# Kernel optimization log

Measured on AMD Instinct MI355X. Metric: run time of the kernel, lower is better.

The kernel has to match this reference:

```python
import jax, jax.numpy as jnp
import numpy as np

H, W, BS, CIN = 224, 608, 1, 128
CLS = (16, 12, 10)
PAD = (0, 2, 3)
C12 = CLS[0] * CLS[1]            # 192
C123 = C12 * CLS[2]              # 1920
SUPER = 384
CFACT = C123 // SUPER            # 5
PAD_PROJ = 0.1


def _p(key, shape):
    return jax.random.normal(key, shape, dtype=jnp.float32) * 0.05


def setup_inputs() -> dict:
    key = jax.random.key(0)
    ks = iter(jax.random.split(key, 32))
    d = {"x_in": jax.random.normal(next(ks), (BS, CIN, H, W), dtype=jnp.float32)}
    # stage-1: grouped 1x1 convs (groups=height -> one [out,in] matmul per image line)
    for i, (ci, co) in enumerate([(32, 32), (32, 32), (32, CLS[0] + 2 * PAD[0])]):
        d[f"w1_{i}"] = _p(next(ks), (H, co, ci))
        d[f"b1_{i}"] = _p(next(ks), (H, co))
    # stage-2: CondMul tables indexed by line*16 + stage-1 class
    for i, (ci, co) in enumerate([(32, 32), (32, 32), (32, CLS[1] + 2 * PAD[1])]):
        d[f"w2_{i}"] = _p(next(ks), (H * CLS[0], ci, co))
        d[f"b2_{i}"] = _p(next(ks), (H * CLS[0], co))
    # stage-3: CondMul tables indexed by line*192 + stage-12 class
    for i, (ci, co) in enumerate([(32, 32), (32, 32), (32, CLS[2] + 2 * PAD[2])]):
        d[f"w3_{i}"] = _p(next(ks), (H * C12, ci, co))
        d[f"b3_{i}"] = _p(next(ks), (H * C12, co))
    d["wr0"] = _p(next(ks), (H * SUPER, 32, 32))
    d["br0"] = _p(next(ks), (H * SUPER, 32))
    d["wr1"] = _p(next(ks), (H * C123, 32, 1))
    d["br1"] = _p(next(ks), (H * C123, 1))
    return d


def _condmul(x, inds, w, b):
    # CondMul: y[n] = x[n] @ w[inds[n]] + b[inds[n]]
    return jnp.einsum('ni,nio->no', x, w[inds]) + b[inds]


def _forward(x_in, w1, b1, w2, b2, w3, b3, wr0, br0, wr1, br1):
    bs, _, h, w_ = x_in.shape
    lrelu = jax.nn.leaky_relu  # negative_slope=0.01, same as torch default
    offsets = jnp.arange(h, dtype=jnp.int32).reshape(1, 1, h, 1)
    # ---- stage 1: per-line 1x1 grouped conv stack -> argmax class
    x = x_in[:, 0:32].transpose(0, 2, 1, 3)                    # [b,h,32,w]
    for i in range(3):
        x = jnp.einsum('bhiw,hoi->bhow', x, w1[i]) + b1[i][None, :, :, None]
        if i < 2:
            x = lrelu(x)
    x = x.transpose(0, 2, 1, 3)                                 # [b,16,h,w]
    inds1 = jnp.argmax(x, axis=1)[:, None].astype(jnp.int32)    # [b,1,h,w]
    inds1_l = (inds1 + CLS[0] * offsets).reshape(-1)
    # ---- stage 2: CondMul chain conditioned on (line, class1)
    x = x_in[:, 32:64].transpose(0, 2, 3, 1).reshape(-1, 32)    # [N,32]
    for i in range(3):
        x = _condmul(x, inds1_l, w2[i], b2[i])
        if i < 2:
            x = lrelu(x)
    inds2 = jnp.argmax(x, axis=1).astype(jnp.int32).reshape(bs, 1, h, w_)
    inds12 = inds1 * CLS[1] + (inds2 - PAD[1])
    inds12_l = (jnp.clip(inds12, 0, C12 - 1) + C12 * offsets).reshape(-1)
    # ---- stage 3: CondMul chain conditioned on (line, class12)
    x = x_in[:, 64:96].transpose(0, 2, 3, 1).reshape(-1, 32)
    for i in range(3):
        if i < 2:
            x = lrelu(_condmul(x, inds12_l, w3[i], b3[i]))
        else:
            x = _condmul(x, inds12_l, w3[i], b3[i])
    inds3 = jnp.argmax(x, axis=1).astype(jnp.int32).reshape(bs, 1, h, w_)
    inds123 = jnp.clip(inds12 * CLS[2] + (inds3 - PAD[2]), 0, C123 - 1)
    inds = inds123.reshape(-1)
    lines = jnp.broadcast_to(offsets, (bs, 1, h, w_)).reshape(-1)
    inds_l = inds + C123 * lines                                 # per-leaf index
    inds_super_l = inds // CFACT + SUPER * lines                 # superclass index (reg_line_div=1)
    x = x_in[:, 96:128].transpose(0, 2, 3, 1).reshape(-1, 32)
    x = lrelu(_condmul(x, inds_super_l, wr0, br0))
    r = _condmul(x, inds_l, wr1, br1)[:, 0]                      # [N]
    out = (inds.astype(jnp.float32) + r).reshape(bs, 1, h, w_) / float(C123)
    out = (out - PAD_PROJ) / (1.0 - 2.0 * PAD_PROJ)              # undo projector padding
    return out


def reference(x_in, w1_0, b1_0, w1_1, b1_1, w1_2, b1_2,
              w2_0, b2_0, w2_1, b2_1, w2_2, b2_2,
              w3_0, b3_0, w3_1, b3_1, w3_2, b3_2,
              wr0, br0, wr1, br1):
    return _forward(x_in,
                    (w1_0, w1_1, w1_2), (b1_0, b1_1, b1_2),
                    (w2_0, w2_1, w2_2), (b2_0, b2_1, b2_2),
                    (w3_0, w3_1, w3_2), (b3_0, b3_1, b3_2),
                    wr0, br0, wr1, br1)
```

## Files before the change

kernel.cpp:

```cpp
#include <hip/hip_runtime.h>
#include <cstddef>

#define HH 224
#define WW 608
#define HWSZ (HH * WW)

__device__ __forceinline__ float lrelu(float v) { return v > 0.0f ? v : 0.01f * v; }

template <int CO>
__device__ __forceinline__ void cm4(const float* __restrict__ wmat,
                                    const float* __restrict__ bvec,
                                    int s, const float (&act)[8], float (&acc)[CO / 4]) {
    constexpr int CH = CO / 4;
#pragma unroll
    for (int j = 0; j < CH; j++) acc[j] = 0.0f;
#pragma unroll
    for (int sp = 0; sp < 4; sp++) {
#pragma unroll
        for (int ii = 0; ii < 8; ii++) {
            float xi = __shfl(act[ii], sp, 4);
            const float* wr = wmat + (sp * 8 + ii) * CO + s * CH;
            if constexpr (CH == 8) {
                float4 a = *reinterpret_cast<const float4*>(wr);
                float4 b = *reinterpret_cast<const float4*>(wr + 4);
                acc[0] = fmaf(xi, a.x, acc[0]); acc[1] = fmaf(xi, a.y, acc[1]);
                acc[2] = fmaf(xi, a.z, acc[2]); acc[3] = fmaf(xi, a.w, acc[3]);
                acc[4] = fmaf(xi, b.x, acc[4]); acc[5] = fmaf(xi, b.y, acc[5]);
                acc[6] = fmaf(xi, b.z, acc[6]); acc[7] = fmaf(xi, b.w, acc[7]);
            } else {
                float4 a = *reinterpret_cast<const float4*>(wr);
                acc[0] = fmaf(xi, a.x, acc[0]); acc[1] = fmaf(xi, a.y, acc[1]);
                acc[2] = fmaf(xi, a.z, acc[2]); acc[3] = fmaf(xi, a.w, acc[3]);
            }
        }
    }
#pragma unroll
    for (int j = 0; j < CH; j++) acc[j] += bvec[s * CH + j];
}

__device__ __forceinline__ void wb_lrelu8(float (&act)[8], const float (&acc)[8]) {
#pragma unroll
    for (int j = 0; j < 8; j++) act[j] = lrelu(acc[j]);
}

__device__ __forceinline__ int argmax4(const float (&v)[4], int s) {
    float bv = v[0];
    int bi = 4 * s;
#pragma unroll
    for (int j = 1; j < 4; j++) {
        if (v[j] > bv) { bv = v[j]; bi = 4 * s + j; }
    }
#pragma unroll
    for (int m = 1; m <= 2; m <<= 1) {
        float ov = __shfl_xor(bv, m, 4);
        int oi = __shfl_xor(bi, m, 4);
        if (ov > bv || (ov == bv && oi < bi)) { bv = ov; bi = oi; }
    }
    return bi;
}

extern "C" __global__ __launch_bounds__(256, 4)
void regressor_fused(const float* __restrict__ x_in,
                     const float* __restrict__ w1_0, const float* __restrict__ b1_0,
                     const float* __restrict__ w1_1, const float* __restrict__ b1_1,
                     const float* __restrict__ w1_2, const float* __restrict__ b1_2,
                     const float* __restrict__ w2_0, const float* __restrict__ b2_0,
                     const float* __restrict__ w2_1, const float* __restrict__ b2_1,
                     const float* __restrict__ w2_2, const float* __restrict__ b2_2,
                     const float* __restrict__ w3_0, const float* __restrict__ b3_0,
                     const float* __restrict__ w3_1, const float* __restrict__ b3_1,
                     const float* __restrict__ w3_2, const float* __restrict__ b3_2,
                     const float* __restrict__ wr0, const float* __restrict__ br0,
                     const float* __restrict__ wr1, const float* __restrict__ br1,
                     float* __restrict__ out) {
    const int h = blockIdx.y;
    const int tid = threadIdx.x;
    const int p = tid >> 2;
    const int s = tid & 3;
    const int w = blockIdx.x * 64 + p;
    const bool valid = (w < WW);
    const int wc = valid ? w : (WW - 1);
    const int base = h * WW + wc;

    __shared__ __align__(16) float sW0[1024];
    __shared__ __align__(16) float sW1[1024];
    __shared__ __align__(16) float sW2[512];
    for (int t = tid; t < 1024; t += 256) {
        int i = t >> 5, o = t & 31;
        sW0[t] = w1_0[h * 1024 + o * 32 + i];
        sW1[t] = w1_1[h * 1024 + o * 32 + i];
    }
    for (int t = tid; t < 512; t += 256) {
        int i = t >> 4, o = t & 15;
        sW2[t] = w1_2[h * 512 + o * 32 + i];
    }
    __syncthreads();

    float act[8], acc8[8], acc4[4];

#pragma unroll
    for (int ii = 0; ii < 8; ii++) act[ii] = x_in[(8 * s + ii) * HWSZ + base];
    cm4<32>(sW0, b1_0 + h * 32, s, act, acc8);
    wb_lrelu8(act, acc8);
    cm4<32>(sW1, b1_1 + h * 32, s, act, acc8);
    wb_lrelu8(act, acc8);
    cm4<16>(sW2, b1_2 + h * 16, s, act, acc4);
    const int i1 = argmax4(acc4, s);

#pragma unroll
    for (int ii = 0; ii < 8; ii++) act[ii] = x_in[(32 + 8 * s + ii) * HWSZ + base];
    const size_t idx2 = (size_t)h * 16 + (size_t)i1;
    cm4<32>(w2_0 + idx2 * 1024, b2_0 + idx2 * 32, s, act, acc8);
    wb_lrelu8(act, acc8);
    cm4<32>(w2_1 + idx2 * 1024, b2_1 + idx2 * 32, s, act, acc8);
    wb_lrelu8(act, acc8);
    cm4<16>(w2_2 + idx2 * 512, b2_2 + idx2 * 16, s, act, acc4);
    const int i2 = argmax4(acc4, s);

    const int inds12 = i1 * 12 + (i2 - 2);
    const int c12 = min(max(inds12, 0), 191);
    const size_t idx3 = (size_t)h * 192 + (size_t)c12;

#pragma unroll
    for (int ii = 0; ii < 8; ii++) act[ii] = x_in[(64 + 8 * s + ii) * HWSZ + base];
    cm4<32>(w3_0 + idx3 * 1024, b3_0 + idx3 * 32, s, act, acc8);
    wb_lrelu8(act, acc8);
    cm4<32>(w3_1 + idx3 * 1024, b3_1 + idx3 * 32, s, act, acc8);
    wb_lrelu8(act, acc8);
    cm4<16>(w3_2 + idx3 * 512, b3_2 + idx3 * 16, s, act, acc4);
    const int i3 = argmax4(acc4, s);

    const int inds123 = min(max(inds12 * 10 + (i3 - 3), 0), 1919);

#pragma unroll
    for (int ii = 0; ii < 8; ii++) act[ii] = x_in[(96 + 8 * s + ii) * HWSZ + base];
    const size_t idxs = (size_t)h * 384 + (size_t)(inds123 / 5);
    cm4<32>(wr0 + idxs * 1024, br0 + idxs * 32, s, act, acc8);
    wb_lrelu8(act, acc8);

    const size_t idxr = (size_t)h * 1920 + (size_t)inds123;
    const float* __restrict__ wr1r = wr1 + idxr * 32 + 8 * s;
    float4 wa = *reinterpret_cast<const float4*>(wr1r);
    float4 wb = *reinterpret_cast<const float4*>(wr1r + 4);
    float rpart = 0.0f;
    rpart = fmaf(act[0], wa.x, rpart); rpart = fmaf(act[1], wa.y, rpart);
    rpart = fmaf(act[2], wa.z, rpart); rpart = fmaf(act[3], wa.w, rpart);
    rpart = fmaf(act[4], wb.x, rpart); rpart = fmaf(act[5], wb.y, rpart);
    rpart = fmaf(act[6], wb.z, rpart); rpart = fmaf(act[7], wb.w, rpart);
    rpart += __shfl_xor(rpart, 1, 4);
    rpart += __shfl_xor(rpart, 2, 4);
    const float r = rpart + br1[idxr];

    if (s == 0 && valid) {
        float v = ((float)inds123 + r) * (1.0f / 1920.0f);
        out[h * WW + w] = (v - 0.1f) * 1.25f;
    }
}

extern "C" void kernel_launch(void* const* d_in, const int* in_sizes, int n_in,
                              void* d_out, int out_size, void* d_ws, size_t ws_size,
                              hipStream_t stream) {
    const float* p[23];
    for (int i = 0; i < 23; i++) p[i] = (const float*)d_in[i];
    dim3 grid(10, HH);
    regressor_fused<<<grid, 256, 0, stream>>>(
        p[0],
        p[1], p[2], p[3], p[4], p[5], p[6],
        p[7], p[8], p[9], p[10], p[11], p[12],
        p[13], p[14], p[15], p[16], p[17], p[18],
        p[19], p[20], p[21], p[22],
        (float*)d_out);
}
```

Baseline: 135.2 us.

## Split each pixel across eight lanes instead of four and double grid

Each pixel's 32-channel condmul chain is now spread over eight threads with four channels each, so a block covers 32 pixels and the grid grows from 10 to 19 column blocks (608 = 19*32 exactly, so the bounds check is dropped). This cuts per-thread register use and raises the occupancy hint in the launch bounds from 4 to 8 blocks per CU. Input loads and the output store switch to nontemporal hints. In exchange there are more cross-lane shuffles per matmul and argmax, narrower weight loads, and the shared stage-1 weights are staged into LDS twice as often.

```diff
diff --git a/kernel.cpp b/kernel.cpp
--- a/kernel.cpp
+++ b/kernel.cpp
@@ -8,29 +8,25 @@
 __device__ __forceinline__ float lrelu(float v) { return v > 0.0f ? v : 0.01f * v; }
 
 template <int CO>
-__device__ __forceinline__ void cm4(const float* __restrict__ wmat,
+__device__ __forceinline__ void cm8(const float* __restrict__ wmat,
                                     const float* __restrict__ bvec,
-                                    int s, const float (&act)[8], float (&acc)[CO / 4]) {
-    constexpr int CH = CO / 4;
+                                    int s, const float (&act)[4], float (&acc)[CO / 8]) {
+    constexpr int CH = CO / 8;
 #pragma unroll
     for (int j = 0; j < CH; j++) acc[j] = 0.0f;
 #pragma unroll
-    for (int sp = 0; sp < 4; sp++) {
+    for (int sp = 0; sp < 8; sp++) {
 #pragma unroll
-        for (int ii = 0; ii < 8; ii++) {
-            float xi = __shfl(act[ii], sp, 4);
-            const float* wr = wmat + (sp * 8 + ii) * CO + s * CH;
-            if constexpr (CH == 8) {
-                float4 a = *reinterpret_cast<const float4*>(wr);
-                float4 b = *reinterpret_cast<const float4*>(wr + 4);
-                acc[0] = fmaf(xi, a.x, acc[0]); acc[1] = fmaf(xi, a.y, acc[1]);
-                acc[2] = fmaf(xi, a.z, acc[2]); acc[3] = fmaf(xi, a.w, acc[3]);
-                acc[4] = fmaf(xi, b.x, acc[4]); acc[5] = fmaf(xi, b.y, acc[5]);
-                acc[6] = fmaf(xi, b.z, acc[6]); acc[7] = fmaf(xi, b.w, acc[7]);
-            } else {
+        for (int ii = 0; ii < 4; ii++) {
+            float xi = __shfl(act[ii], sp, 8);
+            const float* wr = wmat + (sp * 4 + ii) * CO + s * CH;
+            if constexpr (CH == 4) {
                 float4 a = *reinterpret_cast<const float4*>(wr);
                 acc[0] = fmaf(xi, a.x, acc[0]); acc[1] = fmaf(xi, a.y, acc[1]);
                 acc[2] = fmaf(xi, a.z, acc[2]); acc[3] = fmaf(xi, a.w, acc[3]);
+            } else {
+                float2 a = *reinterpret_cast<const float2*>(wr);
+                acc[0] = fmaf(xi, a.x, acc[0]); acc[1] = fmaf(xi, a.y, acc[1]);
             }
         }
     }
@@ -38,28 +34,25 @@
     for (int j = 0; j < CH; j++) acc[j] += bvec[s * CH + j];
 }
 
-__device__ __forceinline__ void wb_lrelu8(float (&act)[8], const float (&acc)[8]) {
+__device__ __forceinline__ void wb_lrelu4(float (&act)[4], const float (&acc)[4]) {
 #pragma unroll
-    for (int j = 0; j < 8; j++) act[j] = lrelu(acc[j]);
+    for (int j = 0; j < 4; j++) act[j] = lrelu(acc[j]);
 }
 
-__device__ __forceinline__ int argmax4(const float (&v)[4], int s) {
+__device__ __forceinline__ int argmax8(const float (&v)[2], int s) {
     float bv = v[0];
-    int bi = 4 * s;
+    int bi = 2 * s;
+    if (v[1] > bv) { bv = v[1]; bi = 2 * s + 1; }
 #pragma unroll
-    for (int j = 1; j < 4; j++) {
-        if (v[j] > bv) { bv = v[j]; bi = 4 * s + j; }
-    }
-#pragma unroll
-    for (int m = 1; m <= 2; m <<= 1) {
-        float ov = __shfl_xor(bv, m, 4);
-        int oi = __shfl_xor(bi, m, 4);
+    for (int m = 1; m <= 4; m <<= 1) {
+        float ov = __shfl_xor(bv, m, 8);
+        int oi = __shfl_xor(bi, m, 8);
         if (ov > bv || (ov == bv && oi < bi)) { bv = ov; bi = oi; }
     }
     return bi;
 }
 
-extern "C" __global__ __launch_bounds__(256, 4)
+extern "C" __global__ __launch_bounds__(256, 8)
 void regressor_fused(const float* __restrict__ x_in,
                      const float* __restrict__ w1_0, const float* __restrict__ b1_0,
                      const float* __restrict__ w1_1, const float* __restrict__ b1_1,
@@ -75,12 +68,10 @@
                      float* __restrict__ out) {
     const int h = blockIdx.y;
     const int tid = threadIdx.x;
-    const int p = tid >> 2;
-    const int s = tid & 3;
-    const int w = blockIdx.x * 64 + p;
-    const bool valid = (w < WW);
-    const int wc = valid ? w : (WW - 1);
-    const int base = h * WW + wc;
+    const int p = tid >> 3;
+    const int s = tid & 7;
+    const int w = blockIdx.x * 32 + p;
+    const int base = h * WW + w;
 
     __shared__ __align__(16) float sW0[1024];
     __shared__ __align__(16) float sW1[1024];
@@ -96,64 +87,66 @@
     }
     __syncthreads();
 
-    float act[8], acc8[8], acc4[4];
+    float act[4], acc4[4], acc2[2];
 
 #pragma unroll
-    for (int ii = 0; ii < 8; ii++) act[ii] = x_in[(8 * s + ii) * HWSZ + base];
-    cm4<32>(sW0, b1_0 + h * 32, s, act, acc8);
-    wb_lrelu8(act, acc8);
-    cm4<32>(sW1, b1_1 + h * 32, s, act, acc8);
-    wb_lrelu8(act, acc8);
-    cm4<16>(sW2, b1_2 + h * 16, s, act, acc4);
-    const int i1 = argmax4(acc4, s);
+    for (int ii = 0; ii < 4; ii++)
+        act[ii] = __builtin_nontemporal_load(&x_in[(4 * s + ii) * HWSZ + base]);
+    cm8<32>(sW0, b1_0 + h * 32, s, act, acc4);
+    wb_lrelu4(act, acc4);
+    cm8<32>(sW1, b1_1 + h * 32, s, act, acc4);
+    wb_lrelu4(act, acc4);
+    cm8<16>(sW2, b1_2 + h * 16, s, act, acc2);
+    const int i1 = argmax8(acc2, s);
 
 #pragma unroll
-    for (int ii = 0; ii < 8; ii++) act[ii] = x_in[(32 + 8 * s + ii) * HWSZ + base];
+    for (int ii = 0; ii < 4; ii++)
+        act[ii] = __builtin_nontemporal_load(&x_in[(32 + 4 * s + ii) * HWSZ + base]);
     const size_t idx2 = (size_t)h * 16 + (size_t)i1;
-    cm4<32>(w2_0 + idx2 * 1024, b2_0 + idx2 * 32, s, act, acc8);
-    wb_lrelu8(act, acc8);
-    cm4<32>(w2_1 + idx2 * 1024, b2_1 + idx2 * 32, s, act, acc8);
-    wb_lrelu8(act, acc8);
-    cm4<16>(w2_2 + idx2 * 512, b2_2 + idx2 * 16, s, act, acc4);
-    const int i2 = argmax4(acc4, s);
+    cm8<32>(w2_0 + idx2 * 1024, b2_0 + idx2 * 32, s, act, acc4);
+    wb_lrelu4(act, acc4);
+    cm8<32>(w2_1 + idx2 * 1024, b2_1 + idx2 * 32, s, act, acc4);
+    wb_lrelu4(act, acc4);
+    cm8<16>(w2_2 + idx2 * 512, b2_2 + idx2 * 16, s, act, acc2);
+    const int i2 = argmax8(acc2, s);
 
     const int inds12 = i1 * 12 + (i2 - 2);
     const int c12 = min(max(inds12, 0), 191);
     const size_t idx3 = (size_t)h * 192 + (size_t)c12;
 
 #pragma unroll
-    for (int ii = 0; ii < 8; ii++) act[ii] = x_in[(64 + 8 * s + ii) * HWSZ + base];
-    cm4<32>(w3_0 + idx3 * 1024, b3_0 + idx3 * 32, s, act, acc8);
-    wb_lrelu8(act, acc8);
-    cm4<32>(w3_1 + idx3 * 1024, b3_1 + idx3 * 32, s, act, acc8);
-    wb_lrelu8(act, acc8);
-    cm4<16>(w3_2 + idx3 * 512, b3_2 + idx3 * 16, s, act, acc4);
-    const int i3 = argmax4(acc4, s);
+    for (int ii = 0; ii < 4; ii++)
+        act[ii] = __builtin_nontemporal_load(&x_in[(64 + 4 * s + ii) * HWSZ + base]);
+    cm8<32>(w3_0 + idx3 * 1024, b3_0 + idx3 * 32, s, act, acc4);
+    wb_lrelu4(act, acc4);
+    cm8<32>(w3_1 + idx3 * 1024, b3_1 + idx3 * 32, s, act, acc4);
+    wb_lrelu4(act, acc4);
+    cm8<16>(w3_2 + idx3 * 512, b3_2 + idx3 * 16, s, act, acc2);
+    const int i3 = argmax8(acc2, s);
 
     const int inds123 = min(max(inds12 * 10 + (i3 - 3), 0), 1919);
 
 #pragma unroll
-    for (int ii = 0; ii < 8; ii++) act[ii] = x_in[(96 + 8 * s + ii) * HWSZ + base];
+    for (int ii = 0; ii < 4; ii++)
+        act[ii] = __builtin_nontemporal_load(&x_in[(96 + 4 * s + ii) * HWSZ + base]);
     const size_t idxs = (size_t)h * 384 + (size_t)(inds123 / 5);
-    cm4<32>(wr0 + idxs * 1024, br0 + idxs * 32, s, act, acc8);
-    wb_lrelu8(act, acc8);
+    cm8<32>(wr0 + idxs * 1024, br0 + idxs * 32, s, act, acc4);
+    wb_lrelu4(act, acc4);
 
     const size_t idxr = (size_t)h * 1920 + (size_t)inds123;
-    const float* __restrict__ wr1r = wr1 + idxr * 32 + 8 * s;
+    const float* __restrict__ wr1r = wr1 + idxr * 32 + 4 * s;
     float4 wa = *reinterpret_cast<const float4*>(wr1r);
-    float4 wb = *reinterpret_cast<const float4*>(wr1r + 4);
     float rpart = 0.0f;
     rpart = fmaf(act[0], wa.x, rpart); rpart = fmaf(act[1], wa.y, rpart);
     rpart = fmaf(act[2], wa.z, rpart); rpart = fmaf(act[3], wa.w, rpart);
-    rpart = fmaf(act[4], wb.x, rpart); rpart = fmaf(act[5], wb.y, rpart);
-    rpart = fmaf(act[6], wb.z, rpart); rpart = fmaf(act[7], wb.w, rpart);
-    rpart += __shfl_xor(rpart, 1, 4);
-    rpart += __shfl_xor(rpart, 2, 4);
+    rpart += __shfl_xor(rpart, 1, 8);
+    rpart += __shfl_xor(rpart, 2, 8);
+    rpart += __shfl_xor(rpart, 4, 8);
     const float r = rpart + br1[idxr];
 
-    if (s == 0 && valid) {
+    if (s == 0) {
         float v = ((float)inds123 + r) * (1.0f / 1920.0f);
-        out[h * WW + w] = (v - 0.1f) * 1.25f;
+        __builtin_nontemporal_store((v - 0.1f) * 1.25f, &out[base]);
     }
 }
 
@@ -162,7 +155,7 @@
                               hipStream_t stream) {
     const float* p[23];
     for (int i = 0; i < 23; i++) p[i] = (const float*)d_in[i];
-    dim3 grid(10, HH);
+    dim3 grid(19, HH);
     regressor_fused<<<grid, 256, 0, stream>>>(
         p[0],
         p[1], p[2], p[3], p[4], p[5], p[6],
```

New measurement: 195.2 us. 1.44x slower.

## Prefetch all activation channels upfront and remap blocks across lines

Applied to the files above, without the earlier changes.

All 32 input channels per thread (four stages of 8) are now loaded at kernel start instead of just before each stage, so their latency overlaps the stage-1 compute and the dependent weight gathers. The 2D grid becomes a 1D grid of 2240 blocks whose index is decoded so that 8 consecutive blocks cover 8 different image lines at the same x tile. This is likely meant to spread concurrently running blocks across lines and XCDs, changing cache locality for the per-line weight tables. Holding 24 extra live registers per thread may lower occupancy under launch_bounds(256,4) or cause spills.

```diff
diff --git a/kernel.cpp b/kernel.cpp
--- a/kernel.cpp
+++ b/kernel.cpp
@@ -73,11 +73,17 @@
                      const float* __restrict__ wr0, const float* __restrict__ br0,
                      const float* __restrict__ wr1, const float* __restrict__ br1,
                      float* __restrict__ out) {
-    const int h = blockIdx.y;
+    const int bid = blockIdx.x;
+    const int r = bid & 7;
+    const int t = bid >> 3;
+    const int xblk = t % 10;
+    const int g = t / 10;
+    const int h = 8 * g + r;
+
     const int tid = threadIdx.x;
     const int p = tid >> 2;
     const int s = tid & 3;
-    const int w = blockIdx.x * 64 + p;
+    const int w = xblk * 64 + p;
     const bool valid = (w < WW);
     const int wc = valid ? w : (WW - 1);
     const int base = h * WW + wc;
@@ -85,74 +91,74 @@
     __shared__ __align__(16) float sW0[1024];
     __shared__ __align__(16) float sW1[1024];
     __shared__ __align__(16) float sW2[512];
-    for (int t = tid; t < 1024; t += 256) {
-        int i = t >> 5, o = t & 31;
-        sW0[t] = w1_0[h * 1024 + o * 32 + i];
-        sW1[t] = w1_1[h * 1024 + o * 32 + i];
+    for (int tt = tid; tt < 1024; tt += 256) {
+        int i = tt >> 5, o = tt & 31;
+        sW0[tt] = w1_0[h * 1024 + o * 32 + i];
+        sW1[tt] = w1_1[h * 1024 + o * 32 + i];
     }
-    for (int t = tid; t < 512; t += 256) {
-        int i = t >> 4, o = t & 15;
-        sW2[t] = w1_2[h * 512 + o * 32 + i];
+    for (int tt = tid; tt < 512; tt += 256) {
+        int i = tt >> 4, o = tt & 15;
+        sW2[tt] = w1_2[h * 512 + o * 32 + i];
     }
     __syncthreads();
 
-    float act[8], acc8[8], acc4[4];
+    float act1[8], act2[8], act3[8], actr[8], acc8[8], acc4[4];
 
 #pragma unroll
-    for (int ii = 0; ii < 8; ii++) act[ii] = x_in[(8 * s + ii) * HWSZ + base];
-    cm4<32>(sW0, b1_0 + h * 32, s, act, acc8);
-    wb_lrelu8(act, acc8);
-    cm4<32>(sW1, b1_1 + h * 32, s, act, acc8);
-    wb_lrelu8(act, acc8);
-    cm4<16>(sW2, b1_2 + h * 16, s, act, acc4);
+    for (int ii = 0; ii < 8; ii++) {
+        act1[ii] = x_in[(8 * s + ii) * HWSZ + base];
+        act2[ii] = x_in[(32 + 8 * s + ii) * HWSZ + base];
+        act3[ii] = x_in[(64 + 8 * s + ii) * HWSZ + base];
+        actr[ii] = x_in[(96 + 8 * s + ii) * HWSZ + base];
+    }
+
+    cm4<32>(sW0, b1_0 + h * 32, s, act1, acc8);
+    wb_lrelu8(act1, acc8);
+    cm4<32>(sW1, b1_1 + h * 32, s, act1, acc8);
+    wb_lrelu8(act1, acc8);
+    cm4<16>(sW2, b1_2 + h * 16, s, act1, acc4);
     const int i1 = argmax4(acc4, s);
 
-#pragma unroll
-    for (int ii = 0; ii < 8; ii++) act[ii] = x_in[(32 + 8 * s + ii) * HWSZ + base];
     const size_t idx2 = (size_t)h * 16 + (size_t)i1;
-    cm4<32>(w2_0 + idx2 * 1024, b2_0 + idx2 * 32, s, act, acc8);
-    wb_lrelu8(act, acc8);
-    cm4<32>(w2_1 + idx2 * 1024, b2_1 + idx2 * 32, s, act, acc8);
-    wb_lrelu8(act, acc8);
-    cm4<16>(w2_2 + idx2 * 512, b2_2 + idx2 * 16, s, act, acc4);
+    cm4<32>(w2_0 + idx2 * 1024, b2_0 + idx2 * 32, s, act2, acc8);
+    wb_lrelu8(act2, acc8);
+    cm4<32>(w2_1 + idx2 * 1024, b2_1 + idx2 * 32, s, act2, acc8);
+    wb_lrelu8(act2, acc8);
+    cm4<16>(w2_2 + idx2 * 512, b2_2 + idx2 * 16, s, act2, acc4);
     const int i2 = argmax4(acc4, s);
 
     const int inds12 = i1 * 12 + (i2 - 2);
     const int c12 = min(max(inds12, 0), 191);
     const size_t idx3 = (size_t)h * 192 + (size_t)c12;
 
-#pragma unroll
-    for (int ii = 0; ii < 8; ii++) act[ii] = x_in[(64 + 8 * s + ii) * HWSZ + base];
-    cm4<32>(w3_0 + idx3 * 1024, b3_0 + idx3 * 32, s, act, acc8);
-    wb_lrelu8(act, acc8);
-    cm4<32>(w3_1 + idx3 * 1024, b3_1 + idx3 * 32, s, act, acc8);
-    wb_lrelu8(act, acc8);
-    cm4<16>(w3_2 + idx3 * 512, b3_2 + idx3 * 16, s, act, acc4);
+    cm4<32>(w3_0 + idx3 * 1024, b3_0 + idx3 * 32, s, act3, acc8);
+    wb_lrelu8(act3, acc8);
+    cm4<32>(w3_1 + idx3 * 1024, b3_1 + idx3 * 32, s, act3, acc8);
+    wb_lrelu8(act3, acc8);
+    cm4<16>(w3_2 + idx3 * 512, b3_2 + idx3 * 16, s, act3, acc4);
     const int i3 = argmax4(acc4, s);
 
     const int inds123 = min(max(inds12 * 10 + (i3 - 3), 0), 1919);
 
-#pragma unroll
-    for (int ii = 0; ii < 8; ii++) act[ii] = x_in[(96 + 8 * s + ii) * HWSZ + base];
     const size_t idxs = (size_t)h * 384 + (size_t)(inds123 / 5);
-    cm4<32>(wr0 + idxs * 1024, br0 + idxs * 32, s, act, acc8);
-    wb_lrelu8(act, acc8);
+    cm4<32>(wr0 + idxs * 1024, br0 + idxs * 32, s, actr, acc8);
+    wb_lrelu8(actr, acc8);
 
     const size_t idxr = (size_t)h * 1920 + (size_t)inds123;
     const float* __restrict__ wr1r = wr1 + idxr * 32 + 8 * s;
     float4 wa = *reinterpret_cast<const float4*>(wr1r);
     float4 wb = *reinterpret_cast<const float4*>(wr1r + 4);
     float rpart = 0.0f;
-    rpart = fmaf(act[0], wa.x, rpart); rpart = fmaf(act[1], wa.y, rpart);
-    rpart = fmaf(act[2], wa.z, rpart); rpart = fmaf(act[3], wa.w, rpart);
-    rpart = fmaf(act[4], wb.x, rpart); rpart = fmaf(act[5], wb.y, rpart);
-    rpart = fmaf(act[6], wb.z, rpart); rpart = fmaf(act[7], wb.w, rpart);
+    rpart = fmaf(actr[0], wa.x, rpart); rpart = fmaf(actr[1], wa.y, rpart);
+    rpart = fmaf(actr[2], wa.z, rpart); rpart = fmaf(actr[3], wa.w, rpart);
+    rpart = fmaf(actr[4], wb.x, rpart); rpart = fmaf(actr[5], wb.y, rpart);
+    rpart = fmaf(actr[6], wb.z, rpart); rpart = fmaf(actr[7], wb.w, rpart);
     rpart += __shfl_xor(rpart, 1, 4);
     rpart += __shfl_xor(rpart, 2, 4);
-    const float r = rpart + br1[idxr];
+    const float rr = rpart + br1[idxr];
 
     if (s == 0 && valid) {
-        float v = ((float)inds123 + r) * (1.0f / 1920.0f);
+        float v = ((float)inds123 + rr) * (1.0f / 1920.0f);
         out[h * WW + w] = (v - 0.1f) * 1.25f;
     }
 }
@@ -162,8 +168,7 @@
                               hipStream_t stream) {
     const float* p[23];
     for (int i = 0; i < 23; i++) p[i] = (const float*)d_in[i];
-    dim3 grid(10, HH);
-    regressor_fused<<<grid, 256, 0, stream>>>(
+    regressor_fused<<<dim3(2240), 256, 0, stream>>>(
         p[0],
         p[1], p[2], p[3], p[4], p[5], p[6],
         p[7], p[8], p[9], p[10], p[11], p[12],
```

Result: no change. 137.7 us (+1.8%).

## Split fused kernel into stages with per-line class sorting for coherent weight gathers

Applied to the files above, without the earlier changes.

Splits the single fused kernel into three stage kernels and adds a per-line counting sort after stage 1 and stage 2. Pixels are then handled in class-sorted order, so neighbouring threads in a wave read the same CondMul weight tables, which is meant to cut divergent, scattered weight gathers. The cost is five launches, intermediate index arrays in workspace, and non-coalesced x_in reads and output writes through the permutation. The old fused kernel stays as a fallback when the workspace is too small.

```diff
diff --git a/kernel.cpp b/kernel.cpp
--- a/kernel.cpp
+++ b/kernel.cpp
@@ -60,6 +60,163 @@
 }
 
 extern "C" __global__ __launch_bounds__(256, 4)
+void k_stage1(const float* __restrict__ x_in,
+              const float* __restrict__ w1_0, const float* __restrict__ b1_0,
+              const float* __restrict__ w1_1, const float* __restrict__ b1_1,
+              const float* __restrict__ w1_2, const float* __restrict__ b1_2,
+              int* __restrict__ c1out) {
+    const int h = blockIdx.y;
+    const int tid = threadIdx.x;
+    const int p = tid >> 2;
+    const int s = tid & 3;
+    const int w = blockIdx.x * 64 + p;
+    const bool valid = (w < WW);
+    const int wc = valid ? w : (WW - 1);
+    const int base = h * WW + wc;
+
+    __shared__ __align__(16) float sW0[1024];
+    __shared__ __align__(16) float sW1[1024];
+    __shared__ __align__(16) float sW2[512];
+    for (int tt = tid; tt < 1024; tt += 256) {
+        int i = tt >> 5, o = tt & 31;
+        sW0[tt] = w1_0[h * 1024 + o * 32 + i];
+        sW1[tt] = w1_1[h * 1024 + o * 32 + i];
+    }
+    for (int tt = tid; tt < 512; tt += 256) {
+        int i = tt >> 4, o = tt & 15;
+        sW2[tt] = w1_2[h * 512 + o * 32 + i];
+    }
+    __syncthreads();
+
+    float act[8], acc8[8], acc4[4];
+#pragma unroll
+    for (int ii = 0; ii < 8; ii++) act[ii] = x_in[(8 * s + ii) * HWSZ + base];
+    cm4<32>(sW0, b1_0 + h * 32, s, act, acc8);
+    wb_lrelu8(act, acc8);
+    cm4<32>(sW1, b1_1 + h * 32, s, act, acc8);
+    wb_lrelu8(act, acc8);
+    cm4<16>(sW2, b1_2 + h * 16, s, act, acc4);
+    const int i1 = argmax4(acc4, s);
+
+    if (s == 0 && valid) c1out[base] = i1;
+}
+
+template <int NBINS>
+__global__ __launch_bounds__(256)
+void k_sort(const int* __restrict__ cls_in, int* __restrict__ perm, int clipmax) {
+    const int h = blockIdx.x;
+    const int tid = threadIdx.x;
+    __shared__ int cls[WW];
+    __shared__ int off[NBINS];
+    __shared__ int hist[NBINS];
+    for (int t = tid; t < NBINS; t += 256) hist[t] = 0;
+    __syncthreads();
+    for (int t = tid; t < WW; t += 256) {
+        int v = cls_in[h * WW + t];
+        v = min(max(v, 0), clipmax);
+        cls[t] = v;
+        atomicAdd(&hist[v], 1);
+    }
+    __syncthreads();
+    if (tid == 0) {
+        int run = 0;
+        for (int i = 0; i < NBINS; i++) { off[i] = run; run += hist[i]; }
+    }
+    __syncthreads();
+    for (int t = tid; t < WW; t += 256) {
+        int pos = atomicAdd(&off[cls[t]], 1);
+        perm[h * WW + pos] = t;
+    }
+}
+
+extern "C" __global__ __launch_bounds__(256, 4)
+void k_stage2(const float* __restrict__ x_in,
+              const float* __restrict__ w2_0, const float* __restrict__ b2_0,
+              const float* __restrict__ w2_1, const float* __restrict__ b2_1,
+              const float* __restrict__ w2_2, const float* __restrict__ b2_2,
+              const int* __restrict__ c1arr, const int* __restrict__ perm1,
+              int* __restrict__ inds12out) {
+    const int h = blockIdx.y;
+    const int tid = threadIdx.x;
+    const int s = tid & 3;
+    int pos = blockIdx.x * 64 + (tid >> 2);
+    pos = min(pos, WW - 1);
+    const int p = perm1[h * WW + pos];
+    const int base = h * WW + p;
+    const int i1 = c1arr[base];
+
+    float act[8], acc8[8], acc4[4];
+#pragma unroll
+    for (int ii = 0; ii < 8; ii++) act[ii] = x_in[(32 + 8 * s + ii) * HWSZ + base];
+    const size_t idx2 = (size_t)h * 16 + (size_t)i1;
+    cm4<32>(w2_0 + idx2 * 1024, b2_0 + idx2 * 32, s, act, acc8);
+    wb_lrelu8(act, acc8);
+    cm4<32>(w2_1 + idx2 * 1024, b2_1 + idx2 * 32, s, act, acc8);
+    wb_lrelu8(act, acc8);
+    cm4<16>(w2_2 + idx2 * 512, b2_2 + idx2 * 16, s, act, acc4);
+    const int i2 = argmax4(acc4, s);
+
+    if (s == 0) inds12out[base] = i1 * 12 + (i2 - 2);
+}
+
+extern "C" __global__ __launch_bounds__(256, 4)
+void k_stage3(const float* __restrict__ x_in,
+              const float* __restrict__ w3_0, const float* __restrict__ b3_0,
+              const float* __restrict__ w3_1, const float* __restrict__ b3_1,
+              const float* __restrict__ w3_2, const float* __restrict__ b3_2,
+              const float* __restrict__ wr0, const float* __restrict__ br0,
+              const float* __restrict__ wr1, const float* __restrict__ br1,
+              const int* __restrict__ inds12arr, const int* __restrict__ perm2,
+              float* __restrict__ out) {
+    const int h = blockIdx.y;
+    const int tid = threadIdx.x;
+    const int s = tid & 3;
+    int pos = blockIdx.x * 64 + (tid >> 2);
+    pos = min(pos, WW - 1);
+    const int p = perm2[h * WW + pos];
+    const int base = h * WW + p;
+    const int inds12 = inds12arr[base];
+    const int c12 = min(max(inds12, 0), 191);
+    const size_t idx3 = (size_t)h * 192 + (size_t)c12;
+
+    float act[8], acc8[8], acc4[4];
+#pragma unroll
+    for (int ii = 0; ii < 8; ii++) act[ii] = x_in[(64 + 8 * s + ii) * HWSZ + base];
+    cm4<32>(w3_0 + idx3 * 1024, b3_0 + idx3 * 32, s, act, acc8);
+    wb_lrelu8(act, acc8);
+    cm4<32>(w3_1 + idx3 * 1024, b3_1 + idx3 * 32, s, act, acc8);
+    wb_lrelu8(act, acc8);
+    cm4<16>(w3_2 + idx3 * 512, b3_2 + idx3 * 16, s, act, acc4);
+    const int i3 = argmax4(acc4, s);
+
+    const int inds123 = min(max(inds12 * 10 + (i3 - 3), 0), 1919);
+
+#pragma unroll
+    for (int ii = 0; ii < 8; ii++) act[ii] = x_in[(96 + 8 * s + ii) * HWSZ + base];
+    const size_t idxs = (size_t)h * 384 + (size_t)(inds123 / 5);
+    cm4<32>(wr0 + idxs * 1024, br0 + idxs * 32, s, act, acc8);
+    wb_lrelu8(act, acc8);
+
+    const size_t idxr = (size_t)h * 1920 + (size_t)inds123;
+    const float* __restrict__ wr1r = wr1 + idxr * 32 + 8 * s;
+    float4 wa = *reinterpret_cast<const float4*>(wr1r);
+    float4 wb = *reinterpret_cast<const float4*>(wr1r + 4);
+    float rpart = 0.0f;
+    rpart = fmaf(act[0], wa.x, rpart); rpart = fmaf(act[1], wa.y, rpart);
+    rpart = fmaf(act[2], wa.z, rpart); rpart = fmaf(act[3], wa.w, rpart);
+    rpart = fmaf(act[4], wb.x, rpart); rpart = fmaf(act[5], wb.y, rpart);
+    rpart = fmaf(act[6], wb.z, rpart); rpart = fmaf(act[7], wb.w, rpart);
+    rpart += __shfl_xor(rpart, 1, 4);
+    rpart += __shfl_xor(rpart, 2, 4);
+    const float r = rpart + br1[idxr];
+
+    if (s == 0) {
+        float v = ((float)inds123 + r) * (1.0f / 1920.0f);
+        out[base] = (v - 0.1f) * 1.25f;
+    }
+}
+
+extern "C" __global__ __launch_bounds__(256, 4)
 void regressor_fused(const float* __restrict__ x_in,
                      const float* __restrict__ w1_0, const float* __restrict__ b1_0,
                      const float* __restrict__ w1_1, const float* __restrict__ b1_1,
@@ -85,19 +242,18 @@
     __shared__ __align__(16) float sW0[1024];
     __shared__ __align__(16) float sW1[1024];
     __shared__ __align__(16) float sW2[512];
-    for (int t = tid; t < 1024; t += 256) {
-        int i = t >> 5, o = t & 31;
-        sW0[t] = w1_0[h * 1024 + o * 32 + i];
-        sW1[t] = w1_1[h * 1024 + o * 32 + i];
-    }
-    for (int t = tid; t < 512; t += 256) {
-        int i = t >> 4, o = t & 15;
-        sW2[t] = w1_2[h * 512 + o * 32 + i];
+    for (int tt = tid; tt < 1024; tt += 256) {
+        int i = tt >> 5, o = tt & 31;
+        sW0[tt] = w1_0[h * 1024 + o * 32 + i];
+        sW1[tt] = w1_1[h * 1024 + o * 32 + i];
+    }
+    for (int tt = tid; tt < 512; tt += 256) {
+        int i = tt >> 4, o = tt & 15;
+        sW2[tt] = w1_2[h * 512 + o * 32 + i];
     }
     __syncthreads();
 
     float act[8], acc8[8], acc4[4];
-
 #pragma unroll
     for (int ii = 0; ii < 8; ii++) act[ii] = x_in[(8 * s + ii) * HWSZ + base];
     cm4<32>(sW0, b1_0 + h * 32, s, act, acc8);
@@ -162,12 +318,32 @@
                               hipStream_t stream) {
     const float* p[23];
     for (int i = 0; i < 23; i++) p[i] = (const float*)d_in[i];
-    dim3 grid(10, HH);
-    regressor_fused<<<grid, 256, 0, stream>>>(
-        p[0],
-        p[1], p[2], p[3], p[4], p[5], p[6],
-        p[7], p[8], p[9], p[10], p[11], p[12],
-        p[13], p[14], p[15], p[16], p[17], p[18],
-        p[19], p[20], p[21], p[22],
-        (float*)d_out);
-}
+    float* out = (float*)d_out;
+
+    const size_t N = (size_t)HWSZ;
+    const size_t need = 4 * N * sizeof(int);
+
+    if (ws_size < need) {
+        regressor_fused<<<dim3(10, HH), 256, 0, stream>>>(
+            p[0], p[1], p[2], p[3], p[4], p[5], p[6],
+            p[7], p[8], p[9], p[10], p[11], p[12],
+            p[13], p[14], p[15], p[16], p[17], p[18],
+            p[19], p[20], p[21], p[22], out);
+        return;
+    }
+
+    int* c1 = (int*)d_ws;
+    int* perm1 = c1 + N;
+    int* inds12 = perm1 + N;
+    int* perm2 = inds12 + N;
+
+    dim3 gridMain(10, HH);
+    k_stage1<<<gridMain, 256, 0, stream>>>(p[0], p[1], p[2], p[3], p[4], p[5], p[6], c1);
+    k_sort<16><<<dim3(HH), 256, 0, stream>>>(c1, perm1, 15);
+    k_stage2<<<gridMain, 256, 0, stream>>>(p[0], p[7], p[8], p[9], p[10], p[11], p[12],
+                                           c1, perm1, inds12);
+    k_sort<192><<<dim3(HH), 256, 0, stream>>>(inds12, perm2, 191);
+    k_stage3<<<gridMain, 256, 0, stream>>>(p[0], p[13], p[14], p[15], p[16], p[17], p[18],
+                                           p[19], p[20], p[21], p[22],
+                                           inds12, perm2, out);
+}
```

Measured after the change: 157.5 us. +16.5%, slower.
